# Performance work log

Hardware: AMD Instinct MI355X
Metric: run time of the kernel (lower is better)

The kernel has to match this reference:

```python
import jax, jax.numpy as jnp
import numpy as np

BATCH, N, NX, NU, NY = 64, 4096, 128, 32, 32


def setup_inputs() -> dict:
    key = jax.random.key(0)
    k1, k2, k3, k4, k5 = jax.random.split(key, 5)
    # A scaled to spectral radius ~0.9 so the recurrence is stable (module has is_stable()).
    A = jax.random.normal(k1, (NX, NX), jnp.float32) * (0.9 / np.sqrt(NX).astype(np.float32))
    B = jax.random.normal(k2, (NX, NU), jnp.float32) * (1.0 / np.sqrt(NU).astype(np.float32))
    C = jax.random.normal(k3, (NY, NX), jnp.float32) * (1.0 / np.sqrt(NX).astype(np.float32))
    D = jax.random.normal(k4, (NY, NU), jnp.float32) * (1.0 / np.sqrt(NU).astype(np.float32))
    d = jax.random.normal(k5, (BATCH, N, NU, 1), jnp.float32)
    return {"d": d, "A": A, "B": B, "C": C, "D": D}


def reference(d, A, B, C, D):
    # d: [batch, N, nu, 1]. LTI recurrence: x_{k+1} = A x_k + B u_k ; y_k = C x_k + D u_k, x_0 = 0.
    u = jnp.swapaxes(d[..., 0], 0, 1)  # [N, batch, nu] time-major for scan
    x0 = jnp.zeros((d.shape[0], A.shape[0]), d.dtype)  # [batch, nx]

    def step(x, uk):
        y = x @ C.T + uk @ D.T          # [batch, ny] uses pre-update state x_k
        x_next = x @ A.T + uk @ B.T     # [batch, nx]
        return x_next, (y, x)

    xN, (ys, xs) = jax.lax.scan(step, x0, u)
    y = jnp.swapaxes(ys, 0, 1)[..., None]                      # [batch, N, ny, 1]
    x = jnp.swapaxes(xs, 0, 1)                                 # [batch, N, nx] = x_0..x_{N-1}
    x = jnp.concatenate([x, xN[:, None]], axis=1)[..., None]   # [batch, N+1, nx, 1]
    return y, (x,)
```

## Files before the change

### kernel.cpp

```cpp
#include <hip/hip_runtime.h>
#include <stdint.h>
#include <stddef.h>

typedef short s8v   __attribute__((ext_vector_type(8)));
typedef float f32x4 __attribute__((ext_vector_type(4)));

union BF8 { s8v v; unsigned short u[8]; };

__device__ __forceinline__ void split_trunc(float x, unsigned short &h, unsigned short &l) {
  unsigned u = __builtin_bit_cast(unsigned, x);
  h = (unsigned short)(u >> 16);
  float hi = __builtin_bit_cast(float, u & 0xFFFF0000u);
  float r = x - hi;
  l = (unsigned short)(__builtin_bit_cast(unsigned, r) >> 16);
}
__device__ __forceinline__ f32x4 mfma16(s8v a, s8v b, f32x4 c) {
  return __builtin_amdgcn_mfma_f32_16x16x32_bf16(a, b, c, 0, 0, 0);
}
__device__ __forceinline__ void split8(f32x4 a, f32x4 b, s8v &h, s8v &l) {
  BF8 hh, ll;
  #pragma unroll
  for (int i = 0; i < 4; ++i) { split_trunc(a[i], hh.u[i], ll.u[i]); split_trunc(b[i], hh.u[4 + i], ll.u[4 + i]); }
  h = hh.v; l = ll.v;
}

#define BATCH 64
#define NN    4096
#define NX    128
#define NU    32
#define NY    32
#define LPAD  132
#define CH    32
#define CPB   128

#define OFF_AH   0
#define OFF_AL   32768
#define OFF_BH   65536
#define OFF_BL   73728
#define OFF_CHS  81920
#define OFF_CLS  90112
#define OFF_DH   98304
#define OFF_DL   100352
#define OFF_G1H  102400
#define OFF_G1L  135168
#define OFF_G2H  167936
#define OFF_G2L  200704
#define OFF_G3H  233472
#define OFF_G3L  266240
#define OFF_V    299008
#define OFF_S    4493312
#define OFF_UH   8687616
#define OFF_UL   25464832
#define OFF_KH   42242048
#define OFF_KL   42504192
#define OFF_S5   42766336
#define OFF_PW   43290624

__global__ void k_prep(const float* __restrict__ A, const float* __restrict__ B,
                       const float* __restrict__ C, const float* __restrict__ D,
                       const float* __restrict__ d,
                       unsigned short* Ah, unsigned short* Al,
                       unsigned short* Bh, unsigned short* Bl,
                       unsigned short* Ch, unsigned short* Cl,
                       unsigned short* Dh, unsigned short* Dl,
                       unsigned short* Uh, unsigned short* Ul) {
  const int blk = blockIdx.x;
  if (blk >= 100) {
    const size_t i0 = ((size_t)(blk - 100) * 256 + threadIdx.x) * 8;
    f32x4 a = *(const f32x4*)(d + i0);
    f32x4 b = *(const f32x4*)(d + i0 + 4);
    s8v h, l; split8(a, b, h, l);
    *(s8v*)(Uh + i0) = h;
    *(s8v*)(Ul + i0) = l;
    return;
  }
  int idx = blk * 256 + threadIdx.x;
  unsigned short h, l;
  if (idx < 16384)      { split_trunc(A[idx], h, l); Ah[idx] = h; Al[idx] = l; }
  else if (idx < 20480) { int i = idx - 16384; split_trunc(B[i], h, l); Bh[i] = h; Bl[i] = l; }
  else if (idx < 24576) { int i = idx - 20480; split_trunc(C[i], h, l); Ch[i] = h; Cl[i] = l; }
  else if (idx < 25600) { int i = idx - 24576; split_trunc(D[i], h, l); Dh[i] = h; Dl[i] = l; }
}

__global__ void k_pow0(const float* __restrict__ A, const float* __restrict__ B,
                       float* __restrict__ A2, float* __restrict__ S) {
  const int blk = blockIdx.x;
  if (blk < 64) {
    int gid = blk * 256 + threadIdx.x;
    int row = gid >> 7, col = gid & 127;
    const float* xr = A + row * 128;
    float a0 = 0.f, a1 = 0.f;
    #pragma unroll 8
    for (int k = 0; k < 128; k += 2) {
      a0 = fmaf(xr[k],     A[k * 128 + col],       a0);
      a1 = fmaf(xr[k + 1], A[(k + 1) * 128 + col], a1);
    }
    A2[gid] = a0 + a1;
  } else {
    int gid = (blk - 64) * 256 + threadIdx.x;
    int i = gid >> 5, j = gid & 31;
    S[i * 1024 + j] = B[gid];
    float acc = 0.f;
    #pragma unroll 8
    for (int k = 0; k < 128; ++k) acc = fmaf(A[i * 128 + k], B[k * 32 + j], acc);
    S[i * 1024 + 32 + j] = acc;
  }
}

__global__ void k_powN(const float* __restrict__ X, float* __restrict__ Z,
                       float* __restrict__ S, int half, int sh,
                       unsigned short* Zh, unsigned short* Zl, int writeBF) {
  const int blk = blockIdx.x;
  if (blk < 64) {
    int gid = blk * 256 + threadIdx.x;
    int row = gid >> 7, col = gid & 127;
    const float* xr = X + row * 128;
    float a0 = 0.f, a1 = 0.f;
    #pragma unroll 8
    for (int k = 0; k < 128; k += 2) {
      a0 = fmaf(xr[k],     X[k * 128 + col],       a0);
      a1 = fmaf(xr[k + 1], X[(k + 1) * 128 + col], a1);
    }
    float acc = a0 + a1;
    Z[gid] = acc;
    if (writeBF) { unsigned short h, l; split_trunc(acc, h, l); Zh[gid] = h; Zl[gid] = l; }
  } else {
    int idx = (blk - 64) * 256 + threadIdx.x;
    int i = idx >> sh, c = idx & (half - 1);
    const float* xr = X + i * 128;
    float a0 = 0.f, a1 = 0.f;
    #pragma unroll 8
    for (int k = 0; k < 128; k += 2) {
      a0 = fmaf(xr[k],     S[k * 1024 + c],       a0);
      a1 = fmaf(xr[k + 1], S[(k + 1) * 1024 + c], a1);
    }
    S[i * 1024 + half + c] = a0 + a1;
  }
}

__global__ void k_pow5(const float* __restrict__ A32, float* __restrict__ A64,
                       const float* __restrict__ S,
                       unsigned short* G2h, unsigned short* G2l,
                       unsigned short* Kh, unsigned short* Kl) {
  const int blk = blockIdx.x;
  if (blk < 64) {
    int gid = blk * 256 + threadIdx.x;
    int row = gid >> 7, col = gid & 127;
    const float* xr = A32 + row * 128;
    float a0 = 0.f, a1 = 0.f;
    #pragma unroll 8
    for (int k = 0; k < 128; k += 2) {
      a0 = fmaf(xr[k],     A32[k * 128 + col],       a0);
      a1 = fmaf(xr[k + 1], A32[(k + 1) * 128 + col], a1);
    }
    float acc = a0 + a1;
    A64[gid] = acc;
    unsigned short h, l; split_trunc(acc, h, l);
    G2h[gid] = h; G2l[gid] = l;
  } else {
    int idx = (blk - 64) * 256 + threadIdx.x;
    int i = idx >> 10, kk = idx & 1023;
    int t = kk >> 5, j = kk & 31;
    unsigned short h, l;
    split_trunc(S[i * 1024 + (31 - t) * 32 + j], h, l);
    Kh[idx] = h; Kl[idx] = l;
  }
}

__global__ __launch_bounds__(256, 4) void k_vgemm(
    const unsigned short* __restrict__ Uh, const unsigned short* __restrict__ Ul,
    const unsigned short* __restrict__ Kh, const unsigned short* __restrict__ Kl,
    const float* __restrict__ A64, const float* __restrict__ A32,
    unsigned short* G3h, unsigned short* G3l,
    float* __restrict__ vout) {
  const int g = blockIdx.x;
  const int tid = threadIdx.x;
  if (g >= 512) {
    int gid = (g - 512) * 256 + tid;
    int row = gid >> 7, col = gid & 127;
    const float* xr = A64 + row * 128;
    float a0 = 0.f, a1 = 0.f;
    #pragma unroll 8
    for (int k = 0; k < 128; k += 2) {
      a0 = fmaf(xr[k],     A32[k * 128 + col],       a0);
      a1 = fmaf(xr[k + 1], A32[(k + 1) * 128 + col], a1);
    }
    unsigned short h, l; split_trunc(a0 + a1, h, l);
    G3h[gid] = h; G3l[gid] = l;
    return;
  }
  const int w = tid >> 6, l = tid & 63, q = l >> 4, m = l & 15;
  const int ch = g * 16 + m, b = ch >> 7, chunk = ch & (CPB - 1);
  const size_t ubase = ((size_t)b * NN + chunk * CH) * NU + q * 8;
  const unsigned short* uhb = Uh + ubase;
  const unsigned short* ulb = Ul + ubase;
  const int n0 = (2 * w) * 16 + m, n1 = (2 * w + 1) * 16 + m;
  const unsigned short* kh0 = Kh + n0 * 1024 + q * 8;
  const unsigned short* kl0 = Kl + n0 * 1024 + q * 8;
  const unsigned short* kh1 = Kh + n1 * 1024 + q * 8;
  const unsigned short* kl1 = Kl + n1 * 1024 + q * 8;

  f32x4 a00 = {0,0,0,0}, a01 = {0,0,0,0}, a02 = {0,0,0,0};
  f32x4 a10 = {0,0,0,0}, a11 = {0,0,0,0}, a12 = {0,0,0,0};
  #pragma unroll 4
  for (int t = 0; t < 32; ++t) {
    s8v uh  = *(const s8v*)(uhb + t * 32);
    s8v ul  = *(const s8v*)(ulb + t * 32);
    s8v k0h = *(const s8v*)(kh0 + t * 32);
    s8v k0l = *(const s8v*)(kl0 + t * 32);
    s8v k1h = *(const s8v*)(kh1 + t * 32);
    s8v k1l = *(const s8v*)(kl1 + t * 32);
    a00 = mfma16(uh, k0h, a00);
    a01 = mfma16(ul, k0h, a01);
    a02 = mfma16(uh, k0l, a02);
    a10 = mfma16(uh, k1h, a10);
    a11 = mfma16(ul, k1h, a11);
    a12 = mfma16(uh, k1l, a12);
  }
  f32x4 acc0 = a00 + a01 + a02;
  f32x4 acc1 = a10 + a11 + a12;
  #pragma unroll
  for (int rr = 0; rr < 4; ++rr) {
    const int row = g * 16 + q * 4 + rr;
    vout[(size_t)row * 128 + n0] = acc0[rr];
    vout[(size_t)row * 128 + n1] = acc1[rr];
  }
}

__global__ __launch_bounds__(256, 2) void k_carry(
    const unsigned short* __restrict__ G1h, const unsigned short* __restrict__ G1l,
    const unsigned short* __restrict__ G2h, const unsigned short* __restrict__ G2l,
    const unsigned short* __restrict__ G3h, const unsigned short* __restrict__ G3l,
    const float* __restrict__ v, float* __restrict__ sout) {
  const int tid = threadIdx.x;
  const int w = tid >> 6, l = tid & 63, q = l >> 4, m = l & 15;
  const int g = blockIdx.x;
  const int chm = g * 16 + m, cm = chm & (CPB - 1);

  f32x4 a[2];
  a[0] = (f32x4){0.f,0.f,0.f,0.f};
  a[1] = (f32x4){0.f,0.f,0.f,0.f};

#define CARRY_TERM(GH, GL, DELTA)                                              \
  {                                                                            \
    const s8v zero = {0,0,0,0,0,0,0,0};                                        \
    s8v vh[4], vl[4];                                                          \
    _Pragma("unroll")                                                          \
    for (int kt = 0; kt < 4; ++kt) {                                           \
      if (cm >= DELTA) {                                                       \
        const float* vp = v + (size_t)(chm - DELTA) * NX + kt * 32 + q * 8;    \
        split8(*(const f32x4*)vp, *(const f32x4*)(vp + 4), vh[kt], vl[kt]);    \
      } else { vh[kt] = zero; vl[kt] = zero; }                                 \
    }                                                                          \
    _Pragma("unroll")                                                          \
    for (int t2 = 0; t2 < 2; ++t2) {                                           \
      const int n = (2 * w + t2) * 16 + m;                                     \
      _Pragma("unroll")                                                        \
      for (int kt = 0; kt < 4; ++kt) {                                         \
        const int k0 = kt * 32 + q * 8;                                        \
        s8v gh = *(const s8v*)(GH + n * NX + k0);                              \
        s8v gl = *(const s8v*)(GL + n * NX + k0);                              \
        a[t2] = mfma16(vh[kt], gh, a[t2]);                                     \
        a[t2] = mfma16(vl[kt], gh, a[t2]);                                     \
        a[t2] = mfma16(vh[kt], gl, a[t2]);                                     \
      }                                                                        \
    }                                                                          \
  }

  CARRY_TERM(G1h, G1l, 2)
  CARRY_TERM(G2h, G2l, 3)
  CARRY_TERM(G3h, G3l, 4)
#undef CARRY_TERM

  #pragma unroll
  for (int t2 = 0; t2 < 2; ++t2) {
    const int col = (2 * w + t2) * 16 + m;
    #pragma unroll
    for (int rr = 0; rr < 4; ++rr) {
      const int chr = g * 16 + q * 4 + rr, cr = chr & (CPB - 1);
      float sv = 0.f;
      if (cr >= 1) sv = a[t2][rr] + v[(size_t)(chr - 1) * NX + col];
      sout[(size_t)chr * NX + col] = sv;
    }
  }
}

__global__ __launch_bounds__(256, 2) void k_scan2(
    const unsigned short* __restrict__ Uh, const unsigned short* __restrict__ Ul,
    const float* __restrict__ s,
    const unsigned short* __restrict__ Ah, const unsigned short* __restrict__ Al,
    const unsigned short* __restrict__ Bh, const unsigned short* __restrict__ Bl,
    const unsigned short* __restrict__ Ch, const unsigned short* __restrict__ Cl,
    const unsigned short* __restrict__ Dh, const unsigned short* __restrict__ Dl,
    float* __restrict__ yout, float* __restrict__ xout) {
  __shared__ unsigned short Eh[16][LPAD];
  __shared__ unsigned short El[16][LPAD];
  __shared__ unsigned short Oh[16][LPAD];
  __shared__ unsigned short Ol[16][LPAD];
  const int tid = threadIdx.x;
  const int w = tid >> 6, l = tid & 63, q = l >> 4, m = l & 15;
  const int g = blockIdx.x;

  s8v fAh[2][4], fAl[2][4], fBh[2], fBl[2];
  #pragma unroll
  for (int t2 = 0; t2 < 2; ++t2) {
    const int n = (2 * w + t2) * 16 + m;
    #pragma unroll
    for (int kt = 0; kt < 4; ++kt) {
      const int k0 = kt * 32 + q * 8;
      fAh[t2][kt] = *(const s8v*)(Ah + n * 128 + k0);
      fAl[t2][kt] = *(const s8v*)(Al + n * 128 + k0);
    }
    fBh[t2] = *(const s8v*)(Bh + n * 32 + q * 8);
    fBl[t2] = *(const s8v*)(Bl + n * 32 + q * 8);
  }
  s8v fCh[4], fCl[4], fDh, fDl;
  {
    const int o = (w & 1) * 16 + m;
    #pragma unroll
    for (int kt = 0; kt < 4; ++kt) {
      const int k0 = kt * 32 + q * 8;
      fCh[kt] = *(const s8v*)(Ch + o * 128 + k0);
      fCl[kt] = *(const s8v*)(Cl + o * 128 + k0);
    }
    fDh = *(const s8v*)(Dh + o * 32 + q * 8);
    fDl = *(const s8v*)(Dl + o * 32 + q * 8);
  }

  {
    const int lb = tid >> 4, i0 = (tid & 15) * 8;
    const int chS = g * 16 + lb, bS = chS >> 7, cS = chS & (CPB - 1);
    const float* sp = s + (size_t)chS * 128 + i0;
    f32x4 s0 = *(const f32x4*)sp, s1 = *(const f32x4*)(sp + 4);
    s8v hh, ll;
    split8(s0, s1, hh, ll);
    *(s8v*)&Eh[lb][i0] = hh;
    *(s8v*)&El[lb][i0] = ll;
    float* xp = xout + ((size_t)bS * (NN + 1) + (size_t)cS * CH) * NX + i0;
    *(f32x4*)xp = s0;
    *(f32x4*)(xp + 4) = s1;
  }
  __syncthreads();

  const int ch = g * 16 + m, b = ch >> 7, chunk = ch & (CPB - 1);
  const size_t ubase = ((size_t)b * NN + chunk * CH) * NU + q * 8;
  const unsigned short* uhb = Uh + ubase;
  const unsigned short* ulb = Ul + ubase;

  float* xptr[2][4];
  bool xlast[2][4];
  float* yptr[4];
  #pragma unroll
  for (int t2 = 0; t2 < 2; ++t2) {
    const int col = (2 * w + t2) * 16 + m;
    #pragma unroll
    for (int rr = 0; rr < 4; ++rr) {
      const int chX = g * 16 + q * 4 + rr, bX = chX >> 7, cX = chX & (CPB - 1);
      xptr[t2][rr] = xout + ((size_t)bX * (NN + 1) + (size_t)cX * CH + 1) * NX + col;
      xlast[t2][rr] = (cX == CPB - 1);
    }
  }
  #pragma unroll
  for (int rr = 0; rr < 4; ++rr) {
    const int chY = g * 16 + q * 4 + rr, bY = chY >> 7, cY = chY & (CPB - 1);
    yptr[rr] = yout + ((size_t)bY * NN + (size_t)cY * CH) * NY + (w & 1) * 16 + m;
  }

  s8v u0h = *(const s8v*)(uhb),      u0l = *(const s8v*)(ulb);
  s8v u1h = *(const s8v*)(uhb + NU), u1l = *(const s8v*)(ulb + NU);

  #pragma unroll 1
  for (int r = 0; r < 16; ++r) {
    s8v n0h = u0h, n0l = u0l, n1h = u1h, n1l = u1l;
    if (r < 15) {
      const size_t off = (size_t)(2 * r + 2) * NU;
      n0h = *(const s8v*)(uhb + off);      n0l = *(const s8v*)(ulb + off);
      n1h = *(const s8v*)(uhb + off + NU); n1l = *(const s8v*)(ulb + off + NU);
    }
    s8v fXh[4], fXl[4];
    #pragma unroll
    for (int kt = 0; kt < 4; ++kt) {
      fXh[kt] = *(const s8v*)&Eh[m][kt * 32 + q * 8];
      fXl[kt] = *(const s8v*)&El[m][kt * 32 + q * 8];
    }
    f32x4 xo[2];
    #pragma unroll
    for (int t2 = 0; t2 < 2; ++t2) {
      f32x4 a0 = {0.f,0.f,0.f,0.f}, a1 = {0.f,0.f,0.f,0.f}, a2 = {0.f,0.f,0.f,0.f};
      #pragma unroll
      for (int kt = 0; kt < 4; ++kt) a0 = mfma16(fXh[kt], fAh[t2][kt], a0);
      a0 = mfma16(u0h, fBh[t2], a0);
      #pragma unroll
      for (int kt = 0; kt < 4; ++kt) a1 = mfma16(fXl[kt], fAh[t2][kt], a1);
      a1 = mfma16(u0l, fBh[t2], a1);
      #pragma unroll
      for (int kt = 0; kt < 4; ++kt) a2 = mfma16(fXh[kt], fAl[t2][kt], a2);
      a2 = mfma16(u0h, fBl[t2], a2);
      xo[t2] = a0 + a1 + a2;
    }
    if (w < 2) {
      f32x4 b0 = {0.f,0.f,0.f,0.f}, b1 = {0.f,0.f,0.f,0.f}, b2 = {0.f,0.f,0.f,0.f};
      #pragma unroll
      for (int kt = 0; kt < 4; ++kt) b0 = mfma16(fXh[kt], fCh[kt], b0);
      b0 = mfma16(u0h, fDh, b0);
      #pragma unroll
      for (int kt = 0; kt < 4; ++kt) b1 = mfma16(fXl[kt], fCh[kt], b1);
      b1 = mfma16(u0l, fDh, b1);
      #pragma unroll
      for (int kt = 0; kt < 4; ++kt) b2 = mfma16(fXh[kt], fCl[kt], b2);
      b2 = mfma16(u0h, fDl, b2);
      f32x4 yv = b0 + b1 + b2;
      #pragma unroll
      for (int rr = 0; rr < 4; ++rr) *(yptr[rr]) = yv[rr];
    }
    #pragma unroll
    for (int t2 = 0; t2 < 2; ++t2) {
      const int col = (2 * w + t2) * 16 + m;
      #pragma unroll
      for (int rr = 0; rr < 4; ++rr) {
        *(xptr[t2][rr]) = xo[t2][rr];
        unsigned short h, lo;
        split_trunc(xo[t2][rr], h, lo);
        Oh[q * 4 + rr][col] = h;
        Ol[q * 4 + rr][col] = lo;
      }
    }
    __syncthreads();

    s8v fOh[4], fOl[4];
    #pragma unroll
    for (int kt = 0; kt < 4; ++kt) {
      fOh[kt] = *(const s8v*)&Oh[m][kt * 32 + q * 8];
      fOl[kt] = *(const s8v*)&Ol[m][kt * 32 + q * 8];
    }
    f32x4 xe[2];
    #pragma unroll
    for (int t2 = 0; t2 < 2; ++t2) {
      f32x4 a0 = {0.f,0.f,0.f,0.f}, a1 = {0.f,0.f,0.f,0.f}, a2 = {0.f,0.f,0.f,0.f};
      #pragma unroll
      for (int kt = 0; kt < 4; ++kt) a0 = mfma16(fOh[kt], fAh[t2][kt], a0);
      a0 = mfma16(u1h, fBh[t2], a0);
      #pragma unroll
      for (int kt = 0; kt < 4; ++kt) a1 = mfma16(fOl[kt], fAh[t2][kt], a1);
      a1 = mfma16(u1l, fBh[t2], a1);
      #pragma unroll
      for (int kt = 0; kt < 4; ++kt) a2 = mfma16(fOh[kt], fAl[t2][kt], a2);
      a2 = mfma16(u1h, fBl[t2], a2);
      xe[t2] = a0 + a1 + a2;
    }
    if (w >= 2) {
      f32x4 c0 = {0.f,0.f,0.f,0.f}, c1 = {0.f,0.f,0.f,0.f}, c2 = {0.f,0.f,0.f,0.f};
      #pragma unroll
      for (int kt = 0; kt < 4; ++kt) c0 = mfma16(fOh[kt], fCh[kt], c0);
      c0 = mfma16(u1h, fDh, c0);
      #pragma unroll
      for (int kt = 0; kt < 4; ++kt) c1 = mfma16(fOl[kt], fCh[kt], c1);
      c1 = mfma16(u1l, fDh, c1);
      #pragma unroll
      for (int kt = 0; kt < 4; ++kt) c2 = mfma16(fOh[kt], fCl[kt], c2);
      c2 = mfma16(u1h, fDl, c2);
      f32x4 yv = c0 + c1 + c2;
      #pragma unroll
      for (int rr = 0; rr < 4; ++rr) *(yptr[rr] + NY) = yv[rr];
    }
    #pragma unroll
    for (int t2 = 0; t2 < 2; ++t2) {
      const int col = (2 * w + t2) * 16 + m;
      #pragma unroll
      for (int rr = 0; rr < 4; ++rr) {
        if (r < 15 || xlast[t2][rr]) *(xptr[t2][rr] + NX) = xe[t2][rr];
        unsigned short h, lo;
        split_trunc(xe[t2][rr], h, lo);
        Eh[q * 4 + rr][col] = h;
        El[q * 4 + rr][col] = lo;
      }
    }
    __syncthreads();

    if (r < 15) {
      u0h = n0h; u0l = n0l; u1h = n1h; u1l = n1l;
      #pragma unroll
      for (int t2 = 0; t2 < 2; ++t2)
        #pragma unroll
        for (int rr = 0; rr < 4; ++rr) xptr[t2][rr] += 2 * NX;
      #pragma unroll
      for (int rr = 0; rr < 4; ++rr) yptr[rr] += 2 * NY;
    }
  }
}

extern "C" void kernel_launch(void* const* d_in, const int* in_sizes, int n_in,
                              void* d_out, int out_size, void* d_ws, size_t ws_size,
                              hipStream_t stream) {
  (void)in_sizes; (void)n_in; (void)out_size; (void)ws_size;
  const float* d = (const float*)d_in[0];
  const float* A = (const float*)d_in[1];
  const float* B = (const float*)d_in[2];
  const float* C = (const float*)d_in[3];
  const float* D = (const float*)d_in[4];

  char* ws = (char*)d_ws;
  unsigned short* Ah  = (unsigned short*)(ws + OFF_AH);
  unsigned short* Al  = (unsigned short*)(ws + OFF_AL);
  unsigned short* Bh  = (unsigned short*)(ws + OFF_BH);
  unsigned short* Bl  = (unsigned short*)(ws + OFF_BL);
  unsigned short* Chp = (unsigned short*)(ws + OFF_CHS);
  unsigned short* Clp = (unsigned short*)(ws + OFF_CLS);
  unsigned short* Dhp = (unsigned short*)(ws + OFF_DH);
  unsigned short* Dlp = (unsigned short*)(ws + OFF_DL);
  unsigned short* G1h = (unsigned short*)(ws + OFF_G1H);
  unsigned short* G1l = (unsigned short*)(ws + OFF_G1L);
  unsigned short* G2h = (unsigned short*)(ws + OFF_G2H);
  unsigned short* G2l = (unsigned short*)(ws + OFF_G2L);
  unsigned short* G3h = (unsigned short*)(ws + OFF_G3H);
  unsigned short* G3l = (unsigned short*)(ws + OFF_G3L);
  unsigned short* Uh  = (unsigned short*)(ws + OFF_UH);
  unsigned short* Ul  = (unsigned short*)(ws + OFF_UL);
  unsigned short* Kh  = (unsigned short*)(ws + OFF_KH);
  unsigned short* Kl  = (unsigned short*)(ws + OFF_KL);
  float* S5 = (float*)(ws + OFF_S5);
  float* PW = (float*)(ws + OFF_PW);
  float* V  = (float*)(ws + OFF_V);
  float* S  = (float*)(ws + OFF_S);

  float* A2  = PW;
  float* A4  = PW + 16384;
  float* A8  = PW + 32768;
  float* A16 = PW + 49152;
  float* A32 = PW + 65536;
  float* A64 = PW + 81920;

  float* yout = (float*)d_out;
  float* xout = yout + (size_t)BATCH * NN * NY;

  k_prep<<<4196, 256, 0, stream>>>(A, B, C, D, d,
                                   Ah, Al, Bh, Bl, Chp, Clp, Dhp, Dlp, Uh, Ul);
  k_pow0<<<80, 256, 0, stream>>>(A, B, A2, S5);
  k_powN<<<96, 256, 0, stream>>>(A2, A4, S5, 64, 6, nullptr, nullptr, 0);
  k_powN<<<128, 256, 0, stream>>>(A4, A8, S5, 128, 7, nullptr, nullptr, 0);
  k_powN<<<192, 256, 0, stream>>>(A8, A16, S5, 256, 8, nullptr, nullptr, 0);
  k_powN<<<320, 256, 0, stream>>>(A16, A32, S5, 512, 9, G1h, G1l, 1);
  k_pow5<<<576, 256, 0, stream>>>(A32, A64, S5, G2h, G2l, Kh, Kl);

  k_vgemm<<<576, 256, 0, stream>>>(Uh, Ul, Kh, Kl, A64, A32, G3h, G3l, V);
  k_carry<<<512, 256, 0, stream>>>(G1h, G1l, G2h, G2l, G3h, G3l, V, S);
  k_scan2<<<512, 256, 0, stream>>>(Uh, Ul, S, Ah, Al, Bh, Bl, Chp, Clp, Dhp, Dlp,
                                   yout, xout);
}
```

Before: 319.8 us.

## Split fp32 inputs on the fly instead of materializing bf16 hi/lo copies

Removes the prep pass that split the whole input sequence into bf16 hi/lo arrays. k_vgemm and k_scan2 now load fp32 d directly and split it in registers. The small A/B/C/D splitting is folded into k_pow0 as extra blocks, which saves one kernel launch. Syncthreads are replaced with a lgkmcnt-wait plus raw barrier. This avoids writing and then re-reading about 32MB of bf16 copies, at the cost of extra ALU split work and twice the bytes per load in the consumers.

```diff
diff --git a/kernel.cpp b/kernel.cpp
--- a/kernel.cpp
+++ b/kernel.cpp
@@ -23,6 +23,12 @@
   for (int i = 0; i < 4; ++i) { split_trunc(a[i], hh.u[i], ll.u[i]); split_trunc(b[i], hh.u[4 + i], ll.u[4 + i]); }
   h = hh.v; l = ll.v;
 }
+
+#define LDS_BARRIER() do {                                   \
+    asm volatile("s_waitcnt lgkmcnt(0)" ::: "memory");       \
+    __builtin_amdgcn_s_barrier();                            \
+    __builtin_amdgcn_sched_barrier(0);                       \
+  } while (0)
 
 #define BATCH 64
 #define NN    4096
@@ -49,41 +55,18 @@
 #define OFF_G3L  266240
 #define OFF_V    299008
 #define OFF_S    4493312
-#define OFF_UH   8687616
-#define OFF_UL   25464832
-#define OFF_KH   42242048
-#define OFF_KL   42504192
-#define OFF_S5   42766336
-#define OFF_PW   43290624
-
-__global__ void k_prep(const float* __restrict__ A, const float* __restrict__ B,
+#define OFF_KH   8687616
+#define OFF_KL   8949760
+#define OFF_S5   9211904
+#define OFF_PW   9736192
+
+__global__ void k_pow0(const float* __restrict__ A, const float* __restrict__ B,
                        const float* __restrict__ C, const float* __restrict__ D,
-                       const float* __restrict__ d,
+                       float* __restrict__ A2, float* __restrict__ S,
                        unsigned short* Ah, unsigned short* Al,
                        unsigned short* Bh, unsigned short* Bl,
                        unsigned short* Ch, unsigned short* Cl,
-                       unsigned short* Dh, unsigned short* Dl,
-                       unsigned short* Uh, unsigned short* Ul) {
-  const int blk = blockIdx.x;
-  if (blk >= 100) {
-    const size_t i0 = ((size_t)(blk - 100) * 256 + threadIdx.x) * 8;
-    f32x4 a = *(const f32x4*)(d + i0);
-    f32x4 b = *(const f32x4*)(d + i0 + 4);
-    s8v h, l; split8(a, b, h, l);
-    *(s8v*)(Uh + i0) = h;
-    *(s8v*)(Ul + i0) = l;
-    return;
-  }
-  int idx = blk * 256 + threadIdx.x;
-  unsigned short h, l;
-  if (idx < 16384)      { split_trunc(A[idx], h, l); Ah[idx] = h; Al[idx] = l; }
-  else if (idx < 20480) { int i = idx - 16384; split_trunc(B[i], h, l); Bh[i] = h; Bl[i] = l; }
-  else if (idx < 24576) { int i = idx - 20480; split_trunc(C[i], h, l); Ch[i] = h; Cl[i] = l; }
-  else if (idx < 25600) { int i = idx - 24576; split_trunc(D[i], h, l); Dh[i] = h; Dl[i] = l; }
-}
-
-__global__ void k_pow0(const float* __restrict__ A, const float* __restrict__ B,
-                       float* __restrict__ A2, float* __restrict__ S) {
+                       unsigned short* Dh, unsigned short* Dl) {
   const int blk = blockIdx.x;
   if (blk < 64) {
     int gid = blk * 256 + threadIdx.x;
@@ -96,7 +79,7 @@
       a1 = fmaf(xr[k + 1], A[(k + 1) * 128 + col], a1);
     }
     A2[gid] = a0 + a1;
-  } else {
+  } else if (blk < 80) {
     int gid = (blk - 64) * 256 + threadIdx.x;
     int i = gid >> 5, j = gid & 31;
     S[i * 1024 + j] = B[gid];
@@ -104,6 +87,13 @@
     #pragma unroll 8
     for (int k = 0; k < 128; ++k) acc = fmaf(A[i * 128 + k], B[k * 32 + j], acc);
     S[i * 1024 + 32 + j] = acc;
+  } else {
+    int idx = (blk - 80) * 256 + threadIdx.x;
+    unsigned short h, l;
+    if (idx < 16384)      { split_trunc(A[idx], h, l); Ah[idx] = h; Al[idx] = l; }
+    else if (idx < 20480) { int i = idx - 16384; split_trunc(B[i], h, l); Bh[i] = h; Bl[i] = l; }
+    else if (idx < 24576) { int i = idx - 20480; split_trunc(C[i], h, l); Ch[i] = h; Cl[i] = l; }
+    else if (idx < 25600) { int i = idx - 24576; split_trunc(D[i], h, l); Dh[i] = h; Dl[i] = l; }
   }
 }
 
@@ -168,7 +158,7 @@
 }
 
 __global__ __launch_bounds__(256, 4) void k_vgemm(
-    const unsigned short* __restrict__ Uh, const unsigned short* __restrict__ Ul,
+    const float* __restrict__ d,
     const unsigned short* __restrict__ Kh, const unsigned short* __restrict__ Kl,
     const float* __restrict__ A64, const float* __restrict__ A32,
     unsigned short* G3h, unsigned short* G3l,
@@ -191,9 +181,7 @@
   }
   const int w = tid >> 6, l = tid & 63, q = l >> 4, m = l & 15;
   const int ch = g * 16 + m, b = ch >> 7, chunk = ch & (CPB - 1);
-  const size_t ubase = ((size_t)b * NN + chunk * CH) * NU + q * 8;
-  const unsigned short* uhb = Uh + ubase;
-  const unsigned short* ulb = Ul + ubase;
+  const float* db = d + ((size_t)b * NN + chunk * CH) * NU + q * 8;
   const int n0 = (2 * w) * 16 + m, n1 = (2 * w + 1) * 16 + m;
   const unsigned short* kh0 = Kh + n0 * 1024 + q * 8;
   const unsigned short* kl0 = Kl + n0 * 1024 + q * 8;
@@ -204,8 +192,9 @@
   f32x4 a10 = {0,0,0,0}, a11 = {0,0,0,0}, a12 = {0,0,0,0};
   #pragma unroll 4
   for (int t = 0; t < 32; ++t) {
-    s8v uh  = *(const s8v*)(uhb + t * 32);
-    s8v ul  = *(const s8v*)(ulb + t * 32);
+    f32x4 c0 = *(const f32x4*)(db + t * 32);
+    f32x4 c1 = *(const f32x4*)(db + t * 32 + 4);
+    s8v uh, ul; split8(c0, c1, uh, ul);
     s8v k0h = *(const s8v*)(kh0 + t * 32);
     s8v k0l = *(const s8v*)(kl0 + t * 32);
     s8v k1h = *(const s8v*)(kh1 + t * 32);
@@ -286,8 +275,7 @@
 }
 
 __global__ __launch_bounds__(256, 2) void k_scan2(
-    const unsigned short* __restrict__ Uh, const unsigned short* __restrict__ Ul,
-    const float* __restrict__ s,
+    const float* __restrict__ d, const float* __restrict__ s,
     const unsigned short* __restrict__ Ah, const unsigned short* __restrict__ Al,
     const unsigned short* __restrict__ Bh, const unsigned short* __restrict__ Bl,
     const unsigned short* __restrict__ Ch, const unsigned short* __restrict__ Cl,
@@ -340,12 +328,10 @@
     *(f32x4*)xp = s0;
     *(f32x4*)(xp + 4) = s1;
   }
-  __syncthreads();
+  LDS_BARRIER();
 
   const int ch = g * 16 + m, b = ch >> 7, chunk = ch & (CPB - 1);
-  const size_t ubase = ((size_t)b * NN + chunk * CH) * NU + q * 8;
-  const unsigned short* uhb = Uh + ubase;
-  const unsigned short* ulb = Ul + ubase;
+  const float* ubase = d + ((size_t)b * NN + chunk * CH) * NU + q * 8;
 
   float* xptr[2][4];
   bool xlast[2][4];
@@ -366,17 +352,20 @@
     yptr[rr] = yout + ((size_t)bY * NN + (size_t)cY * CH) * NY + (w & 1) * 16 + m;
   }
 
-  s8v u0h = *(const s8v*)(uhb),      u0l = *(const s8v*)(ulb);
-  s8v u1h = *(const s8v*)(uhb + NU), u1l = *(const s8v*)(ulb + NU);
+  f32x4 cu[4];
+  cu[0] = *(const f32x4*)(ubase);      cu[1] = *(const f32x4*)(ubase + 4);
+  cu[2] = *(const f32x4*)(ubase + 32); cu[3] = *(const f32x4*)(ubase + 36);
 
   #pragma unroll 1
   for (int r = 0; r < 16; ++r) {
-    s8v n0h = u0h, n0l = u0l, n1h = u1h, n1l = u1l;
+    f32x4 nu0 = cu[0], nu1 = cu[1], nu2 = cu[2], nu3 = cu[3];
     if (r < 15) {
-      const size_t off = (size_t)(2 * r + 2) * NU;
-      n0h = *(const s8v*)(uhb + off);      n0l = *(const s8v*)(ulb + off);
-      n1h = *(const s8v*)(uhb + off + NU); n1l = *(const s8v*)(ulb + off + NU);
-    }
+      const float* up = ubase + (size_t)(2 * r + 2) * NU;
+      nu0 = *(const f32x4*)up;        nu1 = *(const f32x4*)(up + 4);
+      nu2 = *(const f32x4*)(up + 32); nu3 = *(const f32x4*)(up + 36);
+    }
+    s8v u0h, u0l;
+    split8(cu[0], cu[1], u0h, u0l);
     s8v fXh[4], fXl[4];
     #pragma unroll
     for (int kt = 0; kt < 4; ++kt) {
@@ -425,8 +414,10 @@
         Ol[q * 4 + rr][col] = lo;
       }
     }
-    __syncthreads();
-
+    LDS_BARRIER();
+
+    s8v u1h, u1l;
+    split8(cu[2], cu[3], u1h, u1l);
     s8v fOh[4], fOl[4];
     #pragma unroll
     for (int kt = 0; kt < 4; ++kt) {
@@ -475,10 +466,10 @@
         El[q * 4 + rr][col] = lo;
       }
     }
-    __syncthreads();
+    LDS_BARRIER();
 
     if (r < 15) {
-      u0h = n0h; u0l = n0l; u1h = n1h; u1l = n1l;
+      cu[0] = nu0; cu[1] = nu1; cu[2] = nu2; cu[3] = nu3;
       #pragma unroll
       for (int t2 = 0; t2 < 2; ++t2)
         #pragma unroll
@@ -514,8 +505,6 @@
   unsigned short* G2l = (unsigned short*)(ws + OFF_G2L);
   unsigned short* G3h = (unsigned short*)(ws + OFF_G3H);
   unsigned short* G3l = (unsigned short*)(ws + OFF_G3L);
-  unsigned short* Uh  = (unsigned short*)(ws + OFF_UH);
-  unsigned short* Ul  = (unsigned short*)(ws + OFF_UL);
   unsigned short* Kh  = (unsigned short*)(ws + OFF_KH);
   unsigned short* Kl  = (unsigned short*)(ws + OFF_KL);
   float* S5 = (float*)(ws + OFF_S5);
@@ -533,17 +522,16 @@
   float* yout = (float*)d_out;
   float* xout = yout + (size_t)BATCH * NN * NY;
 
-  k_prep<<<4196, 256, 0, stream>>>(A, B, C, D, d,
-                                   Ah, Al, Bh, Bl, Chp, Clp, Dhp, Dlp, Uh, Ul);
-  k_pow0<<<80, 256, 0, stream>>>(A, B, A2, S5);
+  k_pow0<<<180, 256, 0, stream>>>(A, B, C, D, A2, S5,
+                                  Ah, Al, Bh, Bl, Chp, Clp, Dhp, Dlp);
   k_powN<<<96, 256, 0, stream>>>(A2, A4, S5, 64, 6, nullptr, nullptr, 0);
   k_powN<<<128, 256, 0, stream>>>(A4, A8, S5, 128, 7, nullptr, nullptr, 0);
   k_powN<<<192, 256, 0, stream>>>(A8, A16, S5, 256, 8, nullptr, nullptr, 0);
   k_powN<<<320, 256, 0, stream>>>(A16, A32, S5, 512, 9, G1h, G1l, 1);
   k_pow5<<<576, 256, 0, stream>>>(A32, A64, S5, G2h, G2l, Kh, Kl);
 
-  k_vgemm<<<576, 256, 0, stream>>>(Uh, Ul, Kh, Kl, A64, A32, G3h, G3l, V);
+  k_vgemm<<<576, 256, 0, stream>>>(d, Kh, Kl, A64, A32, G3h, G3l, V);
   k_carry<<<512, 256, 0, stream>>>(G1h, G1l, G2h, G2l, G3h, G3l, V, S);
-  k_scan2<<<512, 256, 0, stream>>>(Uh, Ul, S, Ah, Al, Bh, Bl, Chp, Clp, Dhp, Dlp,
+  k_scan2<<<512, 256, 0, stream>>>(d, S, Ah, Al, Bh, Bl, Chp, Clp, Dhp, Dlp,
                                    yout, xout);
 }
```

Measured after the change: 303.3 us. 1.05x faster.
